# Optimization experiments

Measured on AMD Instinct MI355X. Metric: run time of the kernel, lower is better.

The kernel has to match this reference:

```python
import jax, jax.numpy as jnp
import numpy as np

N = 50000   # graph nodes (== num_edges of road network, Embedding vocab)
E = 800000  # message-passing edges
F = 64      # static_feat_dim
H = 256     # hidden_dim
ID = 32     # id_embed_dim
DYN = 16    # dyn_feat_dim
B = 256
T = 128
STEPS = 3   # gcn_iter


def setup_inputs():
    key = jax.random.key(0)
    it = iter(jax.random.split(key, 48))

    def nrm(shape, fan_in):
        return jax.random.normal(next(it), shape, jnp.float32) / np.sqrt(fan_in)

    edge_src = jax.random.randint(next(it), (E,), 0, N)
    edge_dst = jax.random.randint(next(it), (E,), 0, N)
    lengths = jax.random.randint(next(it), (B,), T // 2, T + 1)
    traj = jax.random.randint(next(it), (B, T), 1, N)
    mask = jnp.arange(T)[None, :] < lengths[:, None]
    traj = jnp.where(mask, traj, 0)  # padding idx 0 past length
    x0 = jax.random.normal(next(it), (N, F), jnp.float32)
    dyn_feat = jax.random.normal(next(it), (B, DYN), jnp.float32)
    Din = H + ID + DYN
    z = lambda *s: jnp.zeros(s, jnp.float32)
    inp = dict(
        x0=x0, dyn_feat=dyn_feat,
        Wproj=nrm((F, H), F), bproj=z(H),
        Wz=nrm((F + H, H), F + H), bz=z(H),
        Wr=nrm((F + H, H), F + H), br=z(H),
        Wn=nrm((F + H, H), F + H), bn=z(H),
        id_emb=nrm((N, ID), 1.0).at[0].set(0.0),  # padding_idx=0
        film_W1=nrm((DYN, H), DYN), film_b1=z(H),
        film_W2=nrm((H, 2 * H), H), film_b2=z(2 * H),
        gru_Wi_f=nrm((Din, 3 * H), Din), gru_Wh_f=nrm((H, 3 * H), H),
        gru_bi_f=z(3 * H), gru_bh_f=z(3 * H),
        gru_Wi_b=nrm((Din, 3 * H), Din), gru_Wh_b=nrm((H, 3 * H), H),
        gru_bi_b=z(3 * H), gru_bh_b=z(3 * H),
        ln_g=jnp.ones((2 * H,), jnp.float32), ln_b=z(2 * H),
        attn_W1=nrm((2 * H + DYN, H), 2 * H + DYN), attn_b1=z(H),
        attn_W2=nrm((H, 1), H), attn_b2=z(1),
        gate_W=nrm((4 * H + DYN, 2 * H), 4 * H + DYN), gate_b=z(2 * H),
        fc_W1=nrm((2 * H + DYN, H), 2 * H + DYN), fc_b1=z(H),
        fc_W2=nrm((H, 1), H), fc_b2=z(1),
        traj=traj, lengths=lengths, edge_src=edge_src, edge_dst=edge_dst)
    return inp


def _run_gru(x, mask, Wi, Wh, bi, bh):
    # x: [B,T,D]; mask: [B,T] bool. Returns (outs [B,T,H] zeroed past length,
    # h_last [B,H] = state at last valid step), matching packed torch GRU.
    xg = jnp.einsum('btd,dh->bth', x, Wi) + bi  # precompute input gates
    Hd = Wh.shape[0]

    def step(h, inp):
        gx, m = inp
        gh = h @ Wh + bh
        xr, xz, xn = jnp.split(gx, 3, axis=-1)
        hr, hz, hn = jnp.split(gh, 3, axis=-1)
        r = jax.nn.sigmoid(xr + hr)
        zt = jax.nn.sigmoid(xz + hz)
        n = jnp.tanh(xn + r * hn)
        h_new = (1 - zt) * n + zt * h
        m2 = m[:, None]
        h = jnp.where(m2, h_new, h)
        return h, h * m2

    h0 = jnp.zeros((x.shape[0], Hd), x.dtype)
    h_last, outs = jax.lax.scan(step, h0, (jnp.swapaxes(xg, 0, 1), mask.T))
    return jnp.swapaxes(outs, 0, 1), h_last


def _forward(x0, dyn_feat, Wproj, bproj, Wz, bz, Wr, br, Wn, bn, id_emb,
             film_W1, film_b1, film_W2, film_b2,
             gru_Wi_f, gru_Wh_f, gru_bi_f, gru_bh_f,
             gru_Wi_b, gru_Wh_b, gru_bi_b, gru_bh_b,
             ln_g, ln_b, attn_W1, attn_b1, attn_W2, attn_b2,
             gate_W, gate_b, fc_W1, fc_b1, fc_W2, fc_b2,
             traj, lengths, edge_src, edge_dst):
    # --- GGNN message passing: scatter-add aggregation + gated update ---
    h = jnp.tanh(x0 @ Wproj + bproj)  # [N,H]
    for _ in range(STEPS):
        h_agg = jax.ops.segment_sum(h[edge_src], edge_dst, num_segments=N)
        xc = jnp.concatenate([x0, h_agg], axis=1)
        zg = jax.nn.sigmoid(xc @ Wz + bz)
        rg = jax.nn.sigmoid(xc @ Wr + br)
        h_t = jnp.tanh(jnp.concatenate([x0, rg * h_agg], axis=1) @ Wn + bn)
        h = (1 - zg) * h_agg + zg * h_t
    # --- FiLM-modulated trajectory sequence ---
    x_seq = h[traj]  # [B,T,H]
    film = jnp.tanh((dyn_feat @ film_W1 + film_b1) @ film_W2 + film_b2)
    g, b = jnp.split(film, 2, axis=-1)
    x_seq = x_seq * (1 + g[:, None, :]) + b[:, None, :]
    dyn_exp = jnp.broadcast_to(dyn_feat[:, None, :], (B, T, DYN))
    rnn_in = jnp.concatenate([x_seq, id_emb[traj], dyn_exp], axis=-1)
    mask = jnp.arange(T)[None, :] < lengths[:, None]
    # --- BiGRU over packed (length-masked) sequences ---
    out_f, h_f = _run_gru(rnn_in, mask, gru_Wi_f, gru_Wh_f, gru_bi_f, gru_bh_f)
    rev = jnp.maximum(lengths[:, None] - 1 - jnp.arange(T)[None, :], 0)  # [B,T]
    x_rev = jnp.take_along_axis(rnn_in, rev[..., None], axis=1)
    out_rb, h_b = _run_gru(x_rev, mask, gru_Wi_b, gru_Wh_b, gru_bi_b, gru_bh_b)
    out_b = jnp.take_along_axis(out_rb, rev[..., None], axis=1) * mask[..., None]
    rnn_out = jnp.concatenate([out_f, out_b], axis=-1)  # [B,T,2H]
    h_last = jnp.concatenate([h_f, h_b], axis=1)        # [B,2H]
    mu = h_last.mean(-1, keepdims=True)
    var = ((h_last - mu) ** 2).mean(-1, keepdims=True)
    rnn_last = (h_last - mu) / jnp.sqrt(var + 1e-5) * ln_g + ln_b
    # --- attention pooling over valid steps ---
    score_in = jnp.concatenate([rnn_out, dyn_exp], axis=-1)
    scores = (jnp.tanh(score_in @ attn_W1 + attn_b1) @ attn_W2 + attn_b2)[..., 0]
    scores = jnp.where(traj != 0, scores, -1e9)
    alpha = jax.nn.softmax(scores, axis=1)[..., None]
    context = (rnn_out * alpha).sum(axis=1)
    # --- fusion gate + head ---
    gate_in = jnp.concatenate([context, rnn_last, dyn_feat], axis=1)
    zf = jax.nn.sigmoid(gate_in @ gate_W + gate_b)
    final = zf * context + (1 - zf) * rnn_last
    hfc = jax.nn.gelu(jnp.concatenate([final, dyn_feat], axis=1) @ fc_W1 + fc_b1,
                      approximate=False)
    return (hfc @ fc_W2 + fc_b2)[:, 0]


def reference(x0, dyn_feat, Wproj, bproj, Wz, bz, Wr, br, Wn, bn, id_emb,
              film_W1, film_b1, film_W2, film_b2,
              gru_Wi_f, gru_Wh_f, gru_bi_f, gru_bh_f,
              gru_Wi_b, gru_Wh_b, gru_bi_b, gru_bh_b,
              ln_g, ln_b, attn_W1, attn_b1, attn_W2, attn_b2,
              gate_W, gate_b, fc_W1, fc_b1, fc_W2, fc_b2,
              traj, lengths, edge_src, edge_dst):
    return _forward(x0, dyn_feat, Wproj, bproj, Wz, bz, Wr, br, Wn, bn, id_emb,
                    film_W1, film_b1, film_W2, film_b2,
                    gru_Wi_f, gru_Wh_f, gru_bi_f, gru_bh_f,
                    gru_Wi_b, gru_Wh_b, gru_bi_b, gru_bh_b,
                    ln_g, ln_b, attn_W1, attn_b1, attn_W2, attn_b2,
                    gate_W, gate_b, fc_W1, fc_b1, fc_W2, fc_b2,
                    traj, lengths, edge_src, edge_dst)
```

## Files before the change

kernel.cpp:

```cpp
#include <hip/hip_runtime.h>
#include <hip/hip_fp16.h>
#include <cmath>

#define NN   50000
#define EE   800000
#define FF   64
#define HH   256
#define IDD  32
#define DYNN 16
#define BB   256
#define TT   128
#define DIN  304
#define G3   768
#define NQ   (HH/4)
#define NQG  ((FF+HH)/4)
#define NQX  (DIN/4)

typedef _Float16 h2_t __attribute__((ext_vector_type(2)));
__device__ __forceinline__ float sigf(float x){ return 1.0f/(1.0f+expf(-x)); }
__device__ __forceinline__ float fdot2(__half2 a, __half2 b, float c) {
    return __builtin_amdgcn_fdot2(*reinterpret_cast<h2_t*>(&a),
                                  *reinterpret_cast<h2_t*>(&b), c, false);
}

#define NPB 16
__global__ __launch_bounds__(256) void k_proj(
    const float* __restrict__ x0, const float* __restrict__ Wproj,
    const float* __restrict__ bproj, float* __restrict__ h,
    __half* __restrict__ h16)
{
    __shared__ float xs[NPB][FF];
    int n0 = blockIdx.x * NPB;
    int j  = threadIdx.x;
    for (int i = j; i < NPB*FF; i += 256) {
        int m = i / FF, k = i % FF;
        int n = n0 + m;
        xs[m][k] = (n < NN) ? x0[n*FF + k] : 0.f;
    }
    __syncthreads();
    float acc[NPB];
#pragma unroll
    for (int m = 0; m < NPB; ++m) acc[m] = 0.f;
    for (int k = 0; k < FF; ++k) {
        float w = Wproj[k*HH + j];
#pragma unroll
        for (int m = 0; m < NPB; ++m) acc[m] += xs[m][k]*w;
    }
    float b = bproj[j];
#pragma unroll
    for (int m = 0; m < NPB; ++m) {
        int n = n0 + m;
        if (n < NN) {
            float v = tanhf(acc[m] + b);
            h[(size_t)n*HH + j] = v;
            h16[(size_t)n*HH + j] = __float2half(v);
        }
    }
}

__global__ __launch_bounds__(768) void k_wt2(
    const float* __restrict__ Wh, __half2* __restrict__ Wq)
{
    int q = blockIdx.x;
    int j = threadIdx.x;
    float w0 = Wh[(size_t)(4*q+0)*G3 + j];
    float w1 = Wh[(size_t)(4*q+1)*G3 + j];
    float w2 = Wh[(size_t)(4*q+2)*G3 + j];
    float w3 = Wh[(size_t)(4*q+3)*G3 + j];
    Wq[((size_t)q*G3 + j)*2 + 0] = __floats2half2_rn(w0, w1);
    Wq[((size_t)q*G3 + j)*2 + 1] = __floats2half2_rn(w2, w3);
}

__global__ __launch_bounds__(256) void k_wtg(
    const float* __restrict__ W, float2* __restrict__ Wq)
{
    int q = blockIdx.x;
    int j = threadIdx.x;
    __half2 a = __floats2half2_rn(W[(size_t)(4*q+0)*HH + j], W[(size_t)(4*q+1)*HH + j]);
    __half2 b = __floats2half2_rn(W[(size_t)(4*q+2)*HH + j], W[(size_t)(4*q+3)*HH + j]);
    float2 o;
    reinterpret_cast<__half2*>(&o)[0] = a;
    reinterpret_cast<__half2*>(&o)[1] = b;
    Wq[(size_t)q*HH + j] = o;
}

__global__ __launch_bounds__(768) void k_wti(
    const float* __restrict__ Wi, float2* __restrict__ Wq)
{
    int q = blockIdx.x;
    int j = threadIdx.x;
    __half2 a = __floats2half2_rn(Wi[(size_t)(4*q+0)*G3 + j], Wi[(size_t)(4*q+1)*G3 + j]);
    __half2 b = __floats2half2_rn(Wi[(size_t)(4*q+2)*G3 + j], Wi[(size_t)(4*q+3)*G3 + j]);
    float2 o;
    reinterpret_cast<__half2*>(&o)[0] = a;
    reinterpret_cast<__half2*>(&o)[1] = b;
    Wq[(size_t)q*G3 + j] = o;
}

__global__ __launch_bounds__(256) void k_hist(
    const int* __restrict__ dst, int* __restrict__ cnt)
{
    int e = blockIdx.x*256 + threadIdx.x;
    if (e < EE) atomicAdd(&cnt[dst[e]], 1);
}

__global__ __launch_bounds__(1024) void k_prefix(
    const int* __restrict__ cnt, int* __restrict__ offs)
{
    __shared__ int sm[1024];
    __shared__ int carry;
    int j = threadIdx.x;
    if (j == 0) carry = 0;
    __syncthreads();
    for (int base = 0; base < NN; base += 1024) {
        int v = (base + j < NN) ? cnt[base + j] : 0;
        sm[j] = v; __syncthreads();
        for (int s = 1; s < 1024; s <<= 1) {
            int t = (j >= s) ? sm[j - s] : 0;
            __syncthreads();
            sm[j] += t;
            __syncthreads();
        }
        int inc = sm[j];
        int c = carry;
        if (base + j < NN) offs[base + j] = c + inc - v;
        __syncthreads();
        if (j == 1023) carry = c + sm[1023];
        __syncthreads();
    }
    if (j == 0) offs[NN] = carry;
}

__global__ __launch_bounds__(256) void k_fill(
    const int* __restrict__ src, const int* __restrict__ dst,
    const int* __restrict__ offs, int* __restrict__ cur,
    int* __restrict__ srcb)
{
    int e = blockIdx.x*256 + threadIdx.x;
    if (e < EE) {
        int d = dst[e];
        int p = atomicAdd(&cur[d], 1);
        srcb[offs[d] + p] = src[e];
    }
}

#define APB 4
__global__ __launch_bounds__(256) void k_aggregate(
    const __half* __restrict__ h16, const int* __restrict__ offs,
    const int* __restrict__ srcb, float* __restrict__ hagg)
{
    int w    = threadIdx.x >> 6;
    int lane = threadIdx.x & 63;
    int n = blockIdx.x * APB + w;
    if (n >= NN) return;
    int e0 = offs[n], e1 = offs[n+1];
    float4 acc = {0.f, 0.f, 0.f, 0.f};
    int e = e0;
    for (; e + 4 <= e1; e += 4) {
        int s0 = srcb[e], s1 = srcb[e+1], s2 = srcb[e+2], s3 = srcb[e+3];
        float2 r0 = *reinterpret_cast<const float2*>(&h16[(size_t)s0*HH + lane*4]);
        float2 r1 = *reinterpret_cast<const float2*>(&h16[(size_t)s1*HH + lane*4]);
        float2 r2 = *reinterpret_cast<const float2*>(&h16[(size_t)s2*HH + lane*4]);
        float2 r3 = *reinterpret_cast<const float2*>(&h16[(size_t)s3*HH + lane*4]);
#pragma unroll
        for (int u = 0; u < 4; ++u) {
            float2* rp = (u==0)?&r0:(u==1)?&r1:(u==2)?&r2:&r3;
            float2 a = __half22float2(reinterpret_cast<__half2*>(rp)[0]);
            float2 b = __half22float2(reinterpret_cast<__half2*>(rp)[1]);
            acc.x += a.x; acc.y += a.y; acc.z += b.x; acc.w += b.y;
        }
    }
    for (; e < e1; ++e) {
        int s = srcb[e];
        float2 r = *reinterpret_cast<const float2*>(&h16[(size_t)s*HH + lane*4]);
        float2 a = __half22float2(reinterpret_cast<__half2*>(&r)[0]);
        float2 b = __half22float2(reinterpret_cast<__half2*>(&r)[1]);
        acc.x += a.x; acc.y += a.y; acc.z += b.x; acc.w += b.y;
    }
    *reinterpret_cast<float4*>(&hagg[(size_t)n*HH + lane*4]) = acc;
}

__global__ __launch_bounds__(256) void k_gnn_update(
    const float* __restrict__ x0, const float* __restrict__ hagg,
    const float2* __restrict__ wqz, const float2* __restrict__ wqr,
    const float2* __restrict__ wqn,
    const float* __restrict__ bz, const float* __restrict__ br,
    const float* __restrict__ bn, float* __restrict__ h,
    __half* __restrict__ h16)
{
    __shared__ __align__(16) __half inh[NPB][FF+HH];
    __shared__ __align__(16) __half rhh[NPB][HH];
    __shared__ float hsf[NPB][HH];
    int n0 = blockIdx.x * NPB;
    int j  = threadIdx.x;
    for (int i = j; i < NPB*FF; i += 256) {
        int m = i >> 6, k = i & 63;
        int n = n0 + m;
        inh[m][k] = __float2half((n < NN) ? x0[n*FF + k] : 0.f);
    }
#pragma unroll
    for (int m = 0; m < NPB; ++m) {
        int n = n0 + m;
        float hv = (n < NN) ? hagg[(size_t)n*HH + j] : 0.f;
        hsf[m][j] = hv;
        inh[m][FF + j] = __float2half(hv);
    }
    __syncthreads();

    float az[NPB], ar[NPB];
#pragma unroll
    for (int m = 0; m < NPB; ++m) { az[m] = 0.f; ar[m] = 0.f; }
    for (int q = 0; q < NQG; ++q) {
        float2 wzr = wqz[(size_t)q*HH + j];
        float2 wrr = wqr[(size_t)q*HH + j];
        __half2 wz01 = reinterpret_cast<__half2*>(&wzr)[0];
        __half2 wz23 = reinterpret_cast<__half2*>(&wzr)[1];
        __half2 wr01 = reinterpret_cast<__half2*>(&wrr)[0];
        __half2 wr23 = reinterpret_cast<__half2*>(&wrr)[1];
#pragma unroll
        for (int m = 0; m < NPB; ++m) {
            float2 hraw = *reinterpret_cast<const float2*>(&inh[m][4*q]);
            __half2 h01 = reinterpret_cast<__half2*>(&hraw)[0];
            __half2 h23 = reinterpret_cast<__half2*>(&hraw)[1];
            az[m] = fdot2(h01, wz01, az[m]); az[m] = fdot2(h23, wz23, az[m]);
            ar[m] = fdot2(h01, wr01, ar[m]); ar[m] = fdot2(h23, wr23, ar[m]);
        }
    }
    float bzj = bz[j], brj = br[j];
    float zg[NPB];
#pragma unroll
    for (int m = 0; m < NPB; ++m) {
        zg[m] = sigf(az[m] + bzj);
        float rg = sigf(ar[m] + brj);
        rhh[m][j] = __float2half(rg * hsf[m][j]);
    }
    __syncthreads();
    float an[NPB];
#pragma unroll
    for (int m = 0; m < NPB; ++m) an[m] = 0.f;
    for (int q = 0; q < FF/4; ++q) {
        float2 wnr = wqn[(size_t)q*HH + j];
        __half2 wn01 = reinterpret_cast<__half2*>(&wnr)[0];
        __half2 wn23 = reinterpret_cast<__half2*>(&wnr)[1];
#pragma unroll
        for (int m = 0; m < NPB; ++m) {
            float2 hraw = *reinterpret_cast<const float2*>(&inh[m][4*q]);
            __half2 h01 = reinterpret_cast<__half2*>(&hraw)[0];
            __half2 h23 = reinterpret_cast<__half2*>(&hraw)[1];
            an[m] = fdot2(h01, wn01, an[m]); an[m] = fdot2(h23, wn23, an[m]);
        }
    }
    for (int q = FF/4; q < NQG; ++q) {
        float2 wnr = wqn[(size_t)q*HH + j];
        __half2 wn01 = reinterpret_cast<__half2*>(&wnr)[0];
        __half2 wn23 = reinterpret_cast<__half2*>(&wnr)[1];
#pragma unroll
        for (int m = 0; m < NPB; ++m) {
            float2 hraw = *reinterpret_cast<const float2*>(&rhh[m][4*q - FF]);
            __half2 h01 = reinterpret_cast<__half2*>(&hraw)[0];
            __half2 h23 = reinterpret_cast<__half2*>(&hraw)[1];
            an[m] = fdot2(h01, wn01, an[m]); an[m] = fdot2(h23, wn23, an[m]);
        }
    }
    float bnj = bn[j];
#pragma unroll
    for (int m = 0; m < NPB; ++m) {
        int n = n0 + m;
        if (n < NN) {
            float ht = tanhf(an[m] + bnj);
            float hv = (1.f - zg[m])*hsf[m][j] + zg[m]*ht;
            h[(size_t)n*HH + j] = hv;
            h16[(size_t)n*HH + j] = __float2half(hv);
        }
    }
}

__global__ __launch_bounds__(256) void k_film(
    const float* __restrict__ dyn, const float* __restrict__ W1,
    const float* __restrict__ b1, const float* __restrict__ W2,
    const float* __restrict__ b2, float* __restrict__ film)
{
    __shared__ float t1[HH];
    __shared__ float ds[DYNN];
    int b = blockIdx.x, j = threadIdx.x;
    if (j < DYNN) ds[j] = dyn[b*DYNN + j];
    __syncthreads();
    float acc = b1[j];
    for (int k = 0; k < DYNN; ++k) acc += ds[k]*W1[k*HH + j];
    t1[j] = acc;
    __syncthreads();
    float a0 = b2[j], a1 = b2[HH + j];
    for (int k = 0; k < HH; ++k) {
        float t = t1[k];
        a0 += t * W2[k*2*HH + j];
        a1 += t * W2[k*2*HH + HH + j];
    }
    film[b*2*HH + j]      = tanhf(a0);
    film[b*2*HH + HH + j] = tanhf(a1);
}

#define RPB 16
#define XGBLK ((BB*TT)/RPB)
__global__ __launch_bounds__(256) void k_xg2(
    const float* __restrict__ hfin, const float* __restrict__ id_emb,
    const float* __restrict__ dyn,  const float* __restrict__ film,
    const int* __restrict__ traj,   const int* __restrict__ lengths,
    const float2* __restrict__ Wqi_f, const float* __restrict__ bi_f,
    const float2* __restrict__ Wqi_b, const float* __restrict__ bi_b,
    __half* __restrict__ xg_f, __half* __restrict__ xg_b)
{
    __shared__ __align__(16) __half in[RPB][DIN];
    int dir = blockIdx.x / XGBLK;
    int r0  = (blockIdx.x - dir*XGBLK) * RPB;
    const float2* Wq = dir ? Wqi_b : Wqi_f;
    const float* bi = dir ? bi_b : bi_f;
    __half* xg = dir ? xg_b : xg_f;
    int j  = threadIdx.x;
#pragma unroll
    for (int m = 0; m < RPB; ++m) {
        int r = r0 + m;
        int b = r >> 7, t = r & 127;
        int tt = t;
        if (dir) { int L = lengths[b]; tt = L - 1 - t; if (tt < 0) tt = 0; }
        int idx = traj[b*TT + tt];
        float g  = film[b*2*HH + j];
        float bf = film[b*2*HH + HH + j];
        in[m][j] = __float2half(hfin[(size_t)idx*HH + j]*(1.f + g) + bf);
        if (j < IDD)               in[m][HH + j] = __float2half(id_emb[(size_t)idx*IDD + j]);
        else if (j < IDD + DYNN)   in[m][HH + IDD + (j - IDD)] = __float2half(dyn[b*DYNN + (j - IDD)]);
    }
    __syncthreads();
    float a0[RPB], a1[RPB], a2[RPB];
#pragma unroll
    for (int m = 0; m < RPB; ++m) { a0[m] = 0.f; a1[m] = 0.f; a2[m] = 0.f; }
    for (int q = 0; q < NQX; ++q) {
        float2 w0r = Wq[(size_t)q*G3 + j];
        float2 w1r = Wq[(size_t)q*G3 + HH + j];
        float2 w2r = Wq[(size_t)q*G3 + 2*HH + j];
        __half2 w0a = reinterpret_cast<__half2*>(&w0r)[0];
        __half2 w0b = reinterpret_cast<__half2*>(&w0r)[1];
        __half2 w1a = reinterpret_cast<__half2*>(&w1r)[0];
        __half2 w1b = reinterpret_cast<__half2*>(&w1r)[1];
        __half2 w2a = reinterpret_cast<__half2*>(&w2r)[0];
        __half2 w2b = reinterpret_cast<__half2*>(&w2r)[1];
#pragma unroll
        for (int m = 0; m < RPB; ++m) {
            float2 hraw = *reinterpret_cast<const float2*>(&in[m][4*q]);
            __half2 h01 = reinterpret_cast<__half2*>(&hraw)[0];
            __half2 h23 = reinterpret_cast<__half2*>(&hraw)[1];
            a0[m] = fdot2(h01, w0a, a0[m]); a0[m] = fdot2(h23, w0b, a0[m]);
            a1[m] = fdot2(h01, w1a, a1[m]); a1[m] = fdot2(h23, w1b, a1[m]);
            a2[m] = fdot2(h01, w2a, a2[m]); a2[m] = fdot2(h23, w2b, a2[m]);
        }
    }
    float bi0 = bi[j], bi1 = bi[HH + j], bi2 = bi[2*HH + j];
#pragma unroll
    for (int m = 0; m < RPB; ++m) {
        __half* o = &xg[(size_t)(r0 + m)*G3];
        o[j]        = __float2half(a0[m] + bi0);
        o[HH + j]   = __float2half(a1[m] + bi1);
        o[2*HH + j] = __float2half(a2[m] + bi2);
    }
}

#define NBS 2
#define SCBLK (BB/NBS)
__global__ __launch_bounds__(768, 3) void k_scan2(
    const __half* __restrict__ xg_f, const __half* __restrict__ xg_b,
    const __half2* __restrict__ Wq_f, const float* __restrict__ bh_f,
    const __half2* __restrict__ Wq_b, const float* __restrict__ bh_b,
    const int* __restrict__ lengths,
    float* __restrict__ out_f, float* __restrict__ out_b,
    float* __restrict__ h_last)
{
    __shared__ float hsh[NBS][HH];
    __shared__ __align__(16) __half hshh[NBS][HH];
    __shared__ float gh[NBS][G3];
    int dir  = blockIdx.x / SCBLK;
    int bblk = blockIdx.x - dir*SCBLK;
    const __half* xg = dir ? xg_b : xg_f;
    const __half2* Wq = dir ? Wq_b : Wq_f;
    const float* bh = dir ? bh_b : bh_f;
    float* out = dir ? out_b : out_f;
    int b0 = bblk * NBS;
    int j  = threadIdx.x;
    int m  = j >> 8;
    int jj = j & 255;
    if (j < NBS*HH) { hsh[j >> 8][j & 255] = 0.f; hshh[j >> 8][j & 255] = __float2half(0.f); }
    int L0 = lengths[b0], L1 = lengths[b0 + 1];
    float bhj = bh[j];
    const float2* wqp = reinterpret_cast<const float2*>(Wq) + j;
    float2 wreg[NQ];
#pragma unroll
    for (int q = 0; q < NQ; ++q) wreg[q] = wqp[(size_t)q*G3];
    __syncthreads();
    for (int t = 0; t < TT; ++t) {
        float xrv = 0.f, xzv = 0.f, xnv = 0.f;
        if (j < NBS*HH) {
            const __half* xr = &xg[((size_t)(b0 + m)*TT + t)*G3];
            xrv = __half2float(xr[jj]);
            xzv = __half2float(xr[HH + jj]);
            xnv = __half2float(xr[2*HH + jj]);
        }
        float a0 = bhj, a1 = bhj;
#pragma unroll
        for (int p = 0; p < NQ/2; ++p) {
            float4 h0raw = *reinterpret_cast<const float4*>(&hshh[0][8*p]);
            float4 h1raw = *reinterpret_cast<const float4*>(&hshh[1][8*p]);
            const __half2* h0 = reinterpret_cast<const __half2*>(&h0raw);
            const __half2* h1 = reinterpret_cast<const __half2*>(&h1raw);
            float2 w0 = wreg[2*p], w1 = wreg[2*p+1];
            const __half2* wA = reinterpret_cast<const __half2*>(&w0);
            const __half2* wB = reinterpret_cast<const __half2*>(&w1);
            a0 = fdot2(h0[0], wA[0], a0); a0 = fdot2(h0[1], wA[1], a0);
            a0 = fdot2(h0[2], wB[0], a0); a0 = fdot2(h0[3], wB[1], a0);
            a1 = fdot2(h1[0], wA[0], a1); a1 = fdot2(h1[1], wA[1], a1);
            a1 = fdot2(h1[2], wB[0], a1); a1 = fdot2(h1[3], wB[1], a1);
        }
        gh[0][j] = a0; gh[1][j] = a1;
        __syncthreads();
        if (j < NBS*HH) {
            int b = b0 + m;
            int L = m ? L1 : L0;
            float gr = sigf(xrv + gh[m][jj]);
            float gz = sigf(xzv + gh[m][HH + jj]);
            float gn = tanhf(xnv + gr*gh[m][2*HH + jj]);
            float hold = hsh[m][jj];
            float hnew = (1.f - gz)*gn + gz*hold;
            if (t < L) {
                hsh[m][jj] = hnew;
                hshh[m][jj] = __float2half(hnew);
                if (!dir) out[((size_t)b*TT + t)*HH + jj] = hnew;
                else      out[((size_t)b*TT + (L-1-t))*HH + jj] = hnew;
            } else if (!dir) {
                out[((size_t)b*TT + t)*HH + jj] = 0.f;
            }
        }
        __syncthreads();
    }
    if (j < NBS*HH) {
        int b = b0 + m;
        int L = m ? L1 : L0;
        h_last[b*2*HH + (dir ? HH : 0) + jj] = hsh[m][jj];
        if (dir) {
            for (int t = L; t < TT; ++t) out[((size_t)b*TT + t)*HH + jj] = 0.f;
        }
    }
}

#define SPB 16
#define SCD 528
__global__ __launch_bounds__(256) void k_scores(
    const float* __restrict__ out_f, const float* __restrict__ out_b,
    const float* __restrict__ dyn,   const int* __restrict__ traj,
    const float* __restrict__ W1,    const float* __restrict__ b1,
    const float* __restrict__ W2,    const float* __restrict__ b2,
    float* __restrict__ scores)
{
    __shared__ float in[SPB][SCD];
    __shared__ float part[4][SPB];
    int r0 = blockIdx.x * SPB;
    int j  = threadIdx.x;
    int lane = j & 63, wid = j >> 6;
#pragma unroll
    for (int m = 0; m < SPB; ++m) {
        int r = r0 + m;
        int b = r >> 7;
        in[m][j]      = out_f[(size_t)r*HH + j];
        in[m][HH + j] = out_b[(size_t)r*HH + j];
        if (j < DYNN) in[m][2*HH + j] = dyn[b*DYNN + j];
    }
    __syncthreads();
    float acc[SPB];
#pragma unroll
    for (int m = 0; m < SPB; ++m) acc[m] = 0.f;
    for (int k = 0; k < SCD; ++k) {
        float w = W1[k*HH + j];
#pragma unroll
        for (int m = 0; m < SPB; ++m) acc[m] += in[m][k]*w;
    }
    float b1j = b1[j], w2j = W2[j];
#pragma unroll
    for (int m = 0; m < SPB; ++m) {
        float s = tanhf(acc[m] + b1j) * w2j;
#pragma unroll
        for (int off = 32; off > 0; off >>= 1) s += __shfl_xor(s, off, 64);
        if (lane == 0) part[wid][m] = s;
    }
    __syncthreads();
    if (j < SPB) {
        int r = r0 + j;
        int b = r >> 7, t = r & 127;
        float s = part[0][j] + part[1][j] + part[2][j] + part[3][j];
        scores[r] = (traj[b*TT + t] != 0) ? (s + b2[0]) : -1e9f;
    }
}

__global__ __launch_bounds__(256) void k_context(
    const float* __restrict__ scores, const float* __restrict__ out_f,
    const float* __restrict__ out_b,  float* __restrict__ context)
{
    __shared__ float al[TT];
    __shared__ float red[256];
    int b = blockIdx.x, j = threadIdx.x;
    float s = (j < TT) ? scores[b*TT + j] : -INFINITY;
    red[j] = s; __syncthreads();
    for (int t = 128; t > 0; t >>= 1) { if (j < t) red[j] = fmaxf(red[j], red[j+t]); __syncthreads(); }
    float mx = red[0]; __syncthreads();
    float e = (j < TT) ? expf(s - mx) : 0.f;
    red[j] = e; __syncthreads();
    for (int t = 128; t > 0; t >>= 1) { if (j < t) red[j] += red[j+t]; __syncthreads(); }
    float tot = red[0];
    if (j < TT) al[j] = e / tot;
    __syncthreads();
    float c0 = 0.f, c1 = 0.f;
    for (int t = 0; t < TT; ++t) {
        float a = al[t];
        c0 += a * out_f[((size_t)b*TT + t)*HH + j];
        c1 += a * out_b[((size_t)b*TT + t)*HH + j];
    }
    context[b*2*HH + j]      = c0;
    context[b*2*HH + HH + j] = c1;
}

__global__ __launch_bounds__(256) void k_head(
    const float* __restrict__ h_last, const float* __restrict__ context,
    const float* __restrict__ dyn,    const float* __restrict__ ln_g,
    const float* __restrict__ ln_b,   const float* __restrict__ gate_W,
    const float* __restrict__ gate_b, const float* __restrict__ fc_W1,
    const float* __restrict__ fc_b1,  const float* __restrict__ fc_W2,
    const float* __restrict__ fc_b2,  float* __restrict__ outp)
{
    __shared__ float gi[1040];
    __shared__ float fin[SCD];
    __shared__ float red[256];
    int b = blockIdx.x, j = threadIdx.x;
    float h0 = h_last[b*2*HH + j], h1 = h_last[b*2*HH + HH + j];
    red[j] = h0 + h1; __syncthreads();
    for (int s = 128; s > 0; s >>= 1) { if (j < s) red[j] += red[j+s]; __syncthreads(); }
    float mu = red[0] / 512.f; __syncthreads();
    float d0 = h0 - mu, d1 = h1 - mu;
    red[j] = d0*d0 + d1*d1; __syncthreads();
    for (int s = 128; s > 0; s >>= 1) { if (j < s) red[j] += red[j+s]; __syncthreads(); }
    float inv = rsqrtf(red[0] / 512.f + 1e-5f); __syncthreads();
    gi[2*HH + j]      = d0*inv*ln_g[j]      + ln_b[j];
    gi[2*HH + HH + j] = d1*inv*ln_g[HH + j] + ln_b[HH + j];
    gi[j]      = context[b*2*HH + j];
    gi[HH + j] = context[b*2*HH + HH + j];
    if (j < DYNN) gi[1024 + j] = dyn[b*DYNN + j];
    __syncthreads();
    float a0 = gate_b[j], a1 = gate_b[HH + j];
    for (int k = 0; k < 1040; ++k) {
        float x = gi[k];
        a0 += x * gate_W[k*2*HH + j];
        a1 += x * gate_W[k*2*HH + HH + j];
    }
    float z0 = sigf(a0), z1 = sigf(a1);
    fin[j]      = z0*gi[j]      + (1.f - z0)*gi[2*HH + j];
    fin[HH + j] = z1*gi[HH + j] + (1.f - z1)*gi[2*HH + HH + j];
    if (j < DYNN) fin[2*HH + j] = gi[1024 + j];
    __syncthreads();
    float acc = fc_b1[j];
    for (int k = 0; k < SCD; ++k) acc += fin[k]*fc_W1[k*HH + j];
    float x = acc;
    float hfc = 0.5f * x * (1.f + erff(x * 0.70710678118654752f));
    red[j] = hfc * fc_W2[j]; __syncthreads();
    for (int s = 128; s > 0; s >>= 1) { if (j < s) red[j] += red[j+s]; __syncthreads(); }
    if (j == 0) outp[b] = red[0] + fc_b2[0];
}

extern "C" void kernel_launch(void* const* d_in, const int* in_sizes, int n_in,
                              void* d_out, int out_size, void* d_ws, size_t ws_size,
                              hipStream_t stream)
{
    const float* x0      = (const float*)d_in[0];
    const float* dyn     = (const float*)d_in[1];
    const float* Wproj   = (const float*)d_in[2];
    const float* bproj   = (const float*)d_in[3];
    const float* Wz      = (const float*)d_in[4];
    const float* bz      = (const float*)d_in[5];
    const float* Wr      = (const float*)d_in[6];
    const float* br      = (const float*)d_in[7];
    const float* Wn      = (const float*)d_in[8];
    const float* bn      = (const float*)d_in[9];
    const float* id_emb  = (const float*)d_in[10];
    const float* film_W1 = (const float*)d_in[11];
    const float* film_b1 = (const float*)d_in[12];
    const float* film_W2 = (const float*)d_in[13];
    const float* film_b2 = (const float*)d_in[14];
    const float* gWi_f   = (const float*)d_in[15];
    const float* gWh_f   = (const float*)d_in[16];
    const float* gbi_f   = (const float*)d_in[17];
    const float* gbh_f   = (const float*)d_in[18];
    const float* gWi_b   = (const float*)d_in[19];
    const float* gWh_b   = (const float*)d_in[20];
    const float* gbi_b   = (const float*)d_in[21];
    const float* gbh_b   = (const float*)d_in[22];
    const float* ln_g    = (const float*)d_in[23];
    const float* ln_b    = (const float*)d_in[24];
    const float* attn_W1 = (const float*)d_in[25];
    const float* attn_b1 = (const float*)d_in[26];
    const float* attn_W2 = (const float*)d_in[27];
    const float* attn_b2 = (const float*)d_in[28];
    const float* gate_W  = (const float*)d_in[29];
    const float* gate_b  = (const float*)d_in[30];
    const float* fc_W1   = (const float*)d_in[31];
    const float* fc_b1   = (const float*)d_in[32];
    const float* fc_W2   = (const float*)d_in[33];
    const float* fc_b2   = (const float*)d_in[34];
    const int*   traj    = (const int*)d_in[35];
    const int*   lengths = (const int*)d_in[36];
    const int*   e_src   = (const int*)d_in[37];
    const int*   e_dst   = (const int*)d_in[38];

    float* ws = (float*)d_ws;
    const size_t off_h      = 0;
    const size_t off_hagg   = (size_t)NN*HH;
    const size_t off_xgf    = off_hagg;
    const size_t off_xgb    = off_xgf + (size_t)BB*TT*G3/2;
    const size_t off_outf   = 0;
    const size_t off_outb   = off_xgb + (size_t)BB*TT*G3/2;
    const size_t off_film   = off_outb + (size_t)BB*TT*HH;
    const size_t off_hlast  = off_film + (size_t)BB*2*HH;
    const size_t off_scores = off_hlast + (size_t)BB*2*HH;
    const size_t off_ctx    = off_scores + (size_t)BB*TT;
    const size_t off_wqf    = off_ctx + (size_t)BB*2*HH;
    const size_t off_wqb    = off_wqf + (size_t)NQ*G3*2;
    const size_t off_wqz    = off_wqb + (size_t)NQ*G3*2;
    const size_t off_wqr    = off_wqz + (size_t)NQG*HH*2;
    const size_t off_wqn    = off_wqr + (size_t)NQG*HH*2;
    const size_t off_wif    = off_wqn + (size_t)NQG*HH*2;
    const size_t off_wib    = off_wif + (size_t)NQX*G3*2;
    const size_t off_h16    = 27000000;

    float*   h      = ws + off_h;
    float*   hagg   = ws + off_hagg;
    __half*  xg_f   = (__half*)(ws + off_xgf);
    __half*  xg_b   = (__half*)(ws + off_xgb);
    float*   out_f  = ws + off_outf;
    float*   out_b  = ws + off_outb;
    float*   film   = ws + off_film;
    float*   hlast  = ws + off_hlast;
    float*   scores = ws + off_scores;
    float*   ctx    = ws + off_ctx;
    __half2* wq_f   = (__half2*)(ws + off_wqf);
    __half2* wq_b   = (__half2*)(ws + off_wqb);
    float2*  wqz    = (float2*)(ws + off_wqz);
    float2*  wqr    = (float2*)(ws + off_wqr);
    float2*  wqn    = (float2*)(ws + off_wqn);
    float2*  wqi_f  = (float2*)(ws + off_wif);
    float2*  wqi_b  = (float2*)(ws + off_wib);
    __half*  h16    = (__half*)(ws + off_h16);

    int* cnt  = (int*)(ws + off_hagg + (size_t)NN*HH);
    int* cur  = cnt + NN;
    int* offs = cur + NN;
    int* srcb = offs + NN + 1;

    k_proj<<<(NN + NPB - 1)/NPB, 256, 0, stream>>>(x0, Wproj, bproj, h, h16);

    k_wt2<<<NQ, 768, 0, stream>>>(gWh_f, wq_f);
    k_wt2<<<NQ, 768, 0, stream>>>(gWh_b, wq_b);
    k_wtg<<<NQG, 256, 0, stream>>>(Wz, wqz);
    k_wtg<<<NQG, 256, 0, stream>>>(Wr, wqr);
    k_wtg<<<NQG, 256, 0, stream>>>(Wn, wqn);
    k_wti<<<NQX, 768, 0, stream>>>(gWi_f, wqi_f);
    k_wti<<<NQX, 768, 0, stream>>>(gWi_b, wqi_b);

    hipMemsetAsync(cnt, 0, 2*(size_t)NN*sizeof(int), stream);
    k_hist<<<(EE + 255)/256, 256, 0, stream>>>(e_dst, cnt);
    k_prefix<<<1, 1024, 0, stream>>>(cnt, offs);
    k_fill<<<(EE + 255)/256, 256, 0, stream>>>(e_src, e_dst, offs, cur, srcb);

    for (int step = 0; step < 3; ++step) {
        k_aggregate<<<(NN + APB - 1)/APB, 256, 0, stream>>>(h16, offs, srcb, hagg);
        k_gnn_update<<<(NN + NPB - 1)/NPB, 256, 0, stream>>>(
            x0, hagg, wqz, wqr, wqn, bz, br, bn, h, h16);
    }

    k_film<<<BB, 256, 0, stream>>>(dyn, film_W1, film_b1, film_W2, film_b2, film);

    k_xg2<<<2*XGBLK, 256, 0, stream>>>(h, id_emb, dyn, film, traj, lengths,
                                       wqi_f, gbi_f, wqi_b, gbi_b, xg_f, xg_b);

    k_scan2<<<2*SCBLK, 768, 0, stream>>>(xg_f, xg_b, wq_f, gbh_f, wq_b, gbh_b,
                                         lengths, out_f, out_b, hlast);

    k_scores<<<(BB*TT)/SPB, 256, 0, stream>>>(out_f, out_b, dyn, traj,
                                              attn_W1, attn_b1, attn_W2, attn_b2, scores);
    k_context<<<BB, 256, 0, stream>>>(scores, out_f, out_b, ctx);
    k_head<<<BB, 256, 0, stream>>>(hlast, ctx, dyn, ln_g, ln_b, gate_W, gate_b,
                                   fc_W1, fc_b1, fc_W2, fc_b2, (float*)d_out);
}
```

Before: 2.247 ms.

## Widen aggregate gathers to 16B per lane and stage scan weights in LDS

The aggregation kernel now has each half-wavefront gather a whole 256-wide fp16 row with 16-byte loads. Two edges are processed per wave step, and the halves are combined with a cross-half shuffle before the store. The GRU scan kernel no longer keeps all recurrent weights in registers. The first 24 weight rows are staged in shared memory and the rest are read from global memory on every timestep. This lowers register pressure, but it adds LDS traffic and repeated global weight loads inside the serial time loop.

```diff
diff --git a/kernel.cpp b/kernel.cpp
--- a/kernel.cpp
+++ b/kernel.cpp
@@ -151,33 +151,66 @@
 {
     int w    = threadIdx.x >> 6;
     int lane = threadIdx.x & 63;
+    int half = lane >> 5;
+    int l32  = lane & 31;
     int n = blockIdx.x * APB + w;
     if (n >= NN) return;
     int e0 = offs[n], e1 = offs[n+1];
-    float4 acc = {0.f, 0.f, 0.f, 0.f};
+    float acc[8];
+#pragma unroll
+    for (int k = 0; k < 8; ++k) acc[k] = 0.f;
     int e = e0;
-    for (; e + 4 <= e1; e += 4) {
-        int s0 = srcb[e], s1 = srcb[e+1], s2 = srcb[e+2], s3 = srcb[e+3];
-        float2 r0 = *reinterpret_cast<const float2*>(&h16[(size_t)s0*HH + lane*4]);
-        float2 r1 = *reinterpret_cast<const float2*>(&h16[(size_t)s1*HH + lane*4]);
-        float2 r2 = *reinterpret_cast<const float2*>(&h16[(size_t)s2*HH + lane*4]);
-        float2 r3 = *reinterpret_cast<const float2*>(&h16[(size_t)s3*HH + lane*4]);
-#pragma unroll
-        for (int u = 0; u < 4; ++u) {
-            float2* rp = (u==0)?&r0:(u==1)?&r1:(u==2)?&r2:&r3;
-            float2 a = __half22float2(reinterpret_cast<__half2*>(rp)[0]);
-            float2 b = __half22float2(reinterpret_cast<__half2*>(rp)[1]);
-            acc.x += a.x; acc.y += a.y; acc.z += b.x; acc.w += b.y;
-        }
-    }
-    for (; e < e1; ++e) {
+    for (; e + 8 <= e1; e += 8) {
+        int sA = srcb[e     + half];
+        int sB = srcb[e + 2 + half];
+        int sC = srcb[e + 4 + half];
+        int sD = srcb[e + 6 + half];
+        float4 rA = *reinterpret_cast<const float4*>(&h16[(size_t)sA*HH + l32*8]);
+        float4 rB = *reinterpret_cast<const float4*>(&h16[(size_t)sB*HH + l32*8]);
+        float4 rC = *reinterpret_cast<const float4*>(&h16[(size_t)sC*HH + l32*8]);
+        float4 rD = *reinterpret_cast<const float4*>(&h16[(size_t)sD*HH + l32*8]);
+        const __half2* hA = reinterpret_cast<const __half2*>(&rA);
+        const __half2* hB = reinterpret_cast<const __half2*>(&rB);
+        const __half2* hC = reinterpret_cast<const __half2*>(&rC);
+        const __half2* hD = reinterpret_cast<const __half2*>(&rD);
+#pragma unroll
+        for (int k = 0; k < 4; ++k) {
+            float2 a = __half22float2(hA[k]);
+            float2 b = __half22float2(hB[k]);
+            float2 c = __half22float2(hC[k]);
+            float2 d = __half22float2(hD[k]);
+            acc[2*k]   += (a.x + b.x) + (c.x + d.x);
+            acc[2*k+1] += (a.y + b.y) + (c.y + d.y);
+        }
+    }
+    for (; e + 2 <= e1; e += 2) {
+        int s = srcb[e + half];
+        float4 r = *reinterpret_cast<const float4*>(&h16[(size_t)s*HH + l32*8]);
+        const __half2* hp = reinterpret_cast<const __half2*>(&r);
+#pragma unroll
+        for (int k = 0; k < 4; ++k) {
+            float2 a = __half22float2(hp[k]);
+            acc[2*k] += a.x; acc[2*k+1] += a.y;
+        }
+    }
+    if (e < e1 && half == 0) {
         int s = srcb[e];
-        float2 r = *reinterpret_cast<const float2*>(&h16[(size_t)s*HH + lane*4]);
-        float2 a = __half22float2(reinterpret_cast<__half2*>(&r)[0]);
-        float2 b = __half22float2(reinterpret_cast<__half2*>(&r)[1]);
-        acc.x += a.x; acc.y += a.y; acc.z += b.x; acc.w += b.y;
-    }
-    *reinterpret_cast<float4*>(&hagg[(size_t)n*HH + lane*4]) = acc;
+        float4 r = *reinterpret_cast<const float4*>(&h16[(size_t)s*HH + l32*8]);
+        const __half2* hp = reinterpret_cast<const __half2*>(&r);
+#pragma unroll
+        for (int k = 0; k < 4; ++k) {
+            float2 a = __half22float2(hp[k]);
+            acc[2*k] += a.x; acc[2*k+1] += a.y;
+        }
+    }
+#pragma unroll
+    for (int k = 0; k < 8; ++k) acc[k] += __shfl_xor(acc[k], 32, 64);
+    if (half == 0) {
+        float4 o0 = {acc[0], acc[1], acc[2], acc[3]};
+        float4 o1 = {acc[4], acc[5], acc[6], acc[7]};
+        float4* dst = reinterpret_cast<float4*>(&hagg[(size_t)n*HH + l32*8]);
+        dst[0] = o0; dst[1] = o1;
+    }
 }
 
 __global__ __launch_bounds__(256) void k_gnn_update(
@@ -365,6 +398,7 @@
 
 #define NBS 2
 #define SCBLK (BB/NBS)
+#define LQ 24
 __global__ __launch_bounds__(768, 3) void k_scan2(
     const __half* __restrict__ xg_f, const __half* __restrict__ xg_b,
     const __half2* __restrict__ Wq_f, const float* __restrict__ bh_f,
@@ -376,6 +410,7 @@
     __shared__ float hsh[NBS][HH];
     __shared__ __align__(16) __half hshh[NBS][HH];
     __shared__ float gh[NBS][G3];
+    __shared__ __align__(16) float2 lw[LQ][G3];
     int dir  = blockIdx.x / SCBLK;
     int bblk = blockIdx.x - dir*SCBLK;
     const __half* xg = dir ? xg_b : xg_f;
@@ -390,9 +425,8 @@
     int L0 = lengths[b0], L1 = lengths[b0 + 1];
     float bhj = bh[j];
     const float2* wqp = reinterpret_cast<const float2*>(Wq) + j;
-    float2 wreg[NQ];
-#pragma unroll
-    for (int q = 0; q < NQ; ++q) wreg[q] = wqp[(size_t)q*G3];
+#pragma unroll
+    for (int q = 0; q < LQ; ++q) lw[q][j] = wqp[(size_t)q*G3];
     __syncthreads();
     for (int t = 0; t < TT; ++t) {
         float xrv = 0.f, xzv = 0.f, xnv = 0.f;
@@ -404,12 +438,26 @@
         }
         float a0 = bhj, a1 = bhj;
 #pragma unroll
-        for (int p = 0; p < NQ/2; ++p) {
+        for (int p = 0; p < LQ/2; ++p) {
             float4 h0raw = *reinterpret_cast<const float4*>(&hshh[0][8*p]);
             float4 h1raw = *reinterpret_cast<const float4*>(&hshh[1][8*p]);
             const __half2* h0 = reinterpret_cast<const __half2*>(&h0raw);
             const __half2* h1 = reinterpret_cast<const __half2*>(&h1raw);
-            float2 w0 = wreg[2*p], w1 = wreg[2*p+1];
+            float2 w0 = lw[2*p][j], w1 = lw[2*p+1][j];
+            const __half2* wA = reinterpret_cast<const __half2*>(&w0);
+            const __half2* wB = reinterpret_cast<const __half2*>(&w1);
+            a0 = fdot2(h0[0], wA[0], a0); a0 = fdot2(h0[1], wA[1], a0);
+            a0 = fdot2(h0[2], wB[0], a0); a0 = fdot2(h0[3], wB[1], a0);
+            a1 = fdot2(h1[0], wA[0], a1); a1 = fdot2(h1[1], wA[1], a1);
+            a1 = fdot2(h1[2], wB[0], a1); a1 = fdot2(h1[3], wB[1], a1);
+        }
+#pragma unroll
+        for (int p = LQ/2; p < NQ/2; ++p) {
+            float4 h0raw = *reinterpret_cast<const float4*>(&hshh[0][8*p]);
+            float4 h1raw = *reinterpret_cast<const float4*>(&hshh[1][8*p]);
+            const __half2* h0 = reinterpret_cast<const __half2*>(&h0raw);
+            const __half2* h1 = reinterpret_cast<const __half2*>(&h1raw);
+            float2 w0 = wqp[(size_t)(2*p)*G3], w1 = wqp[(size_t)(2*p+1)*G3];
             const __half2* wA = reinterpret_cast<const __half2*>(&w0);
             const __half2* wB = reinterpret_cast<const __half2*>(&w1);
             a0 = fdot2(h0[0], wA[0], a0); a0 = fdot2(h0[1], wA[1], a0);
```

New measurement: 2.306 ms. 1.03x slower.
